# Kernel tuning notes

Measured on AMD Instinct MI355X. Metric: run time of the kernel, lower is better.

## Reference

```python
import jax, jax.numpy as jnp
import numpy as np

M2 = 512  # config['sketch_dim_AV']; seq_len must be divisible by M2


def setup_inputs() -> dict:
    key = jax.random.key(0)
    kq, kk, kv = jax.random.split(key, 3)
    B, H, N, D = 4, 16, 4096, 64
    Q = jax.random.normal(kq, (B, H, N, D), dtype=jnp.float32)
    K = jax.random.normal(kk, (B, H, N, D), dtype=jnp.float32)
    V = jax.random.normal(kv, (B, H, N, D), dtype=jnp.float32)
    mask = jnp.ones((B, N), dtype=jnp.float32)  # unused: self.mask == False
    return {"Q": Q, "K": K, "V": V, "mask": mask}


def reference(Q, K, V, mask):
    # SketchingAttention.forward with sketch_QT=False, method='averaging',
    # sketch_AV=True, use_relu=False, skip_V=True, mask disabled.
    B, H, N, D = Q.shape
    scale = D ** 0.5
    # right_sketch_3D on KS = K.transpose(-1,-2) (shape b,h,d,n):
    # torch does reshape(b*h, d, n) -> reshape(b, h, m2, n//m2, d).mean(-2).
    # Row-major reshape semantics match jnp.reshape exactly, including the
    # intentional (d,n)->(m2, n//m2, d) block reinterpretation.
    SKS = jnp.swapaxes(K, -1, -2).reshape(B, H, M2, N // M2, D).mean(axis=-2)  # (B,H,M2,D)
    # compute_attn(QS, SKS): softmax(Q @ SKS^T / sqrt(d)) over the sketch axis
    logits = jnp.einsum('bhnd,bhmd->bhnm', Q, SKS) / scale  # (B,H,N,M2)
    A_est = jax.nn.softmax(logits, axis=-1)
    # ST_V: chunk-average V along the sequence into M2 buckets
    ST_V = V.reshape(B, H, M2, N // M2, D).mean(axis=-2)  # (B,H,M2,D)
    AV_est = jnp.einsum('bhnm,bhmd->bhnd', A_est, ST_V)
    return AV_est + V  # skip_V residual
```

## Files before the change

### kernel.cpp

```cpp
#include <hip/hip_runtime.h>

using short8 = __attribute__((ext_vector_type(8))) short;
using f32x4  = __attribute__((ext_vector_type(4))) float;

constexpr int NN = 4096;
constexpr int DD = 64;
constexpr int MM = 512;
constexpr int BH = 64;

__device__ __forceinline__ short f2bf(float f) {
    union { float f; unsigned u; } v; v.f = f;
    unsigned r = v.u + 0x7FFF + ((v.u >> 16) & 1);
    return (short)(r >> 16);
}

__global__ __launch_bounds__(1024) void sketch_kernel(
    const float* __restrict__ K, const float* __restrict__ V,
    short* __restrict__ sks, short* __restrict__ stvT) {
    __shared__ float lds[64][65];
    const int t  = threadIdx.x;
    const int lo = t & 63;
    const int hi = t >> 6;
    const int bh = blockIdx.x >> 3;
    const int g  = blockIdx.x & 7;
    const float* Kb = K + ((size_t)bh * NN + g * 512) * DD;
    const float* Vb = V + ((size_t)bh * NN + g * 512) * DD;

#pragma unroll
    for (int i = 0; i < 4; ++i) {
        int e = hi * 4 + i;
        float s = 0.f;
#pragma unroll
        for (int c = 0; c < 8; ++c)
            s += Kb[(size_t)(c * 64 + e) * DD + lo];
        lds[e][lo] = s * 0.125f;
    }
    __syncthreads();
#pragma unroll
    for (int i = 0; i < 4; ++i) {
        int d = hi * 4 + i;
        sks[((size_t)bh * MM + d * 8 + g) * DD + lo] = f2bf(lds[lo][d]);
    }
    __syncthreads();
#pragma unroll
    for (int i = 0; i < 4; ++i) {
        int ml = hi * 4 + i;
        float s = 0.f;
#pragma unroll
        for (int c = 0; c < 8; ++c)
            s += Vb[(size_t)(ml * 8 + c) * DD + lo];
        lds[ml][lo] = s * 0.125f;
    }
    __syncthreads();
#pragma unroll
    for (int i = 0; i < 4; ++i) {
        int e = hi * 4 + i;
        stvT[((size_t)bh * DD + e) * MM + g * 64 + lo] = f2bf(lds[lo][e]);
    }
}

__global__ __launch_bounds__(256, 3) void attn_kernel(
    const float* __restrict__ Q, const float* __restrict__ V,
    const short* __restrict__ sks, const short* __restrict__ stvT,
    float* __restrict__ out) {
    __shared__ __align__(16) short sks_s[64][72];
    __shared__ __align__(16) short stv_s[64][72];
    __shared__ __align__(16) short p_s[4][2][16][72];

    const int tid  = threadIdx.x;
    const int wave = tid >> 6;
    const int lane = tid & 63;
    const int quad = lane >> 4;
    const int l16  = lane & 15;
    const int bh   = blockIdx.x >> 5;
    const int rb   = (blockIdx.x & 31) * 128 + wave * 32;

    const short* sksb = sks + (size_t)bh * MM * DD;
    const short* stvb = stvT + (size_t)bh * DD * MM;

    short8 aq[2][2];
#pragma unroll
    for (int t = 0; t < 2; ++t) {
        const float* qr = Q + ((size_t)bh * NN + rb + t * 16 + l16) * DD;
#pragma unroll
        for (int kc = 0; kc < 2; ++kc)
#pragma unroll
            for (int j = 0; j < 8; ++j)
                aq[t][kc][j] = f2bf(qr[kc * 32 + quad * 8 + j] * 0.125f);
    }

    f32x4 O[2][4];
    float psum[2][4];
#pragma unroll
    for (int t = 0; t < 2; ++t)
#pragma unroll
        for (int nb = 0; nb < 4; ++nb) O[t][nb] = (f32x4){0.f, 0.f, 0.f, 0.f};
#pragma unroll
    for (int t = 0; t < 2; ++t)
#pragma unroll
        for (int r = 0; r < 4; ++r) psum[t][r] = 0.f;

    const int srow = tid >> 2;
    const int scol = (tid & 3) * 16;
    short8 pfk0, pfk1, pfv0, pfv1;
    {
        const short* gk = sksb + (size_t)srow * DD + scol;
        const short* gv = stvb + (size_t)srow * MM + scol;
        pfk0 = *(const short8*)gk;  pfk1 = *(const short8*)(gk + 8);
        pfv0 = *(const short8*)gv;  pfv1 = *(const short8*)(gv + 8);
    }

    for (int mc = 0; mc < 8; ++mc) {
        if (mc) __syncthreads();
        *(short8*)&sks_s[srow][scol]     = pfk0;
        *(short8*)&sks_s[srow][scol + 8] = pfk1;
        *(short8*)&stv_s[srow][scol]     = pfv0;
        *(short8*)&stv_s[srow][scol + 8] = pfv1;
        __syncthreads();
        if (mc < 7) {
            const short* gk = sksb + (size_t)(mc + 1) * 64 * DD + (size_t)srow * DD + scol;
            const short* gv = stvb + (size_t)srow * MM + (mc + 1) * 64 + scol;
            pfk0 = *(const short8*)gk;  pfk1 = *(const short8*)(gk + 8);
            pfv0 = *(const short8*)gv;  pfv1 = *(const short8*)(gv + 8);
        }

        f32x4 S[2][4];
#pragma unroll
        for (int t = 0; t < 2; ++t)
#pragma unroll
            for (int jb = 0; jb < 4; ++jb) S[t][jb] = (f32x4){0.f, 0.f, 0.f, 0.f};
#pragma unroll
        for (int jb = 0; jb < 4; ++jb) {
#pragma unroll
            for (int kc = 0; kc < 2; ++kc) {
                short8 b = *(const short8*)&sks_s[jb * 16 + l16][kc * 32 + quad * 8];
                S[0][jb] = __builtin_amdgcn_mfma_f32_16x16x32_bf16(aq[0][kc], b, S[0][jb], 0, 0, 0);
                S[1][jb] = __builtin_amdgcn_mfma_f32_16x16x32_bf16(aq[1][kc], b, S[1][jb], 0, 0, 0);
            }
        }

#pragma unroll
        for (int t = 0; t < 2; ++t)
#pragma unroll
            for (int jb = 0; jb < 4; ++jb)
#pragma unroll
                for (int r = 0; r < 4; ++r) {
                    float e = __expf(S[t][jb][r]);
                    psum[t][r] += e;
                    p_s[wave][t][quad * 4 + r][jb * 16 + l16] = f2bf(e);
                }

#pragma unroll
        for (int kc = 0; kc < 2; ++kc) {
            short8 a0 = *(const short8*)&p_s[wave][0][l16][kc * 32 + quad * 8];
            short8 a1 = *(const short8*)&p_s[wave][1][l16][kc * 32 + quad * 8];
#pragma unroll
            for (int nb = 0; nb < 4; ++nb) {
                short8 b = *(const short8*)&stv_s[nb * 16 + l16][kc * 32 + quad * 8];
                O[0][nb] = __builtin_amdgcn_mfma_f32_16x16x32_bf16(a0, b, O[0][nb], 0, 0, 0);
                O[1][nb] = __builtin_amdgcn_mfma_f32_16x16x32_bf16(a1, b, O[1][nb], 0, 0, 0);
            }
        }
    }

    float inv[2][4];
#pragma unroll
    for (int t = 0; t < 2; ++t)
#pragma unroll
        for (int r = 0; r < 4; ++r) {
            float s = psum[t][r];
#pragma unroll
            for (int off = 1; off <= 8; off <<= 1)
                s += __shfl_xor(s, off, 64);
            inv[t][r] = 1.0f / s;
        }
#pragma unroll
    for (int t = 0; t < 2; ++t)
#pragma unroll
        for (int nb = 0; nb < 4; ++nb)
#pragma unroll
            for (int r = 0; r < 4; ++r) {
                size_t idx = ((size_t)bh * NN + rb + t * 16 + quad * 4 + r) * DD + nb * 16 + l16;
                out[idx] = O[t][nb][r] * inv[t][r] + V[idx];
            }
}

extern "C" void kernel_launch(void* const* d_in, const int* in_sizes, int n_in,
                              void* d_out, int out_size, void* d_ws, size_t ws_size,
                              hipStream_t stream) {
    const float* Q = (const float*)d_in[0];
    const float* K = (const float*)d_in[1];
    const float* V = (const float*)d_in[2];
    float* out = (float*)d_out;

    short* sks  = (short*)d_ws;
    short* stvT = sks + (size_t)BH * MM * DD;

    sketch_kernel<<<BH * 8, 1024, 0, stream>>>(K, V, sks, stvT);
    attn_kernel<<<BH * (NN / 128), 256, 0, stream>>>(Q, V, sks, stvT, out);
}
```

Measured before the change: 256.3 us.

## Keep softmax probabilities in registers via transposed QK MFMA and permuted STV layout

Computes S transposed by swapping the MFMA operands, so each lane holds consecutive sketch columns for one query row. The exponentials are packed to bf16 with v_cvt_pk_bf16_f32 and fed directly as the A operand of the PV MFMA, which removes the per-wave LDS round trip for P. To match the resulting k ordering, the sketch kernel writes STV^T with a permuted column order. Row sums shrink to two scalars reduced across quads. The launch bound is raised to 4 blocks per CU to allow more occupancy.

```diff
diff --git a/kernel.cpp b/kernel.cpp
--- a/kernel.cpp
+++ b/kernel.cpp
@@ -12,6 +12,12 @@
     union { float f; unsigned u; } v; v.f = f;
     unsigned r = v.u + 0x7FFF + ((v.u >> 16) & 1);
     return (short)(r >> 16);
+}
+
+__device__ __forceinline__ unsigned cvt_pk_bf16(float lo, float hi) {
+    unsigned r;
+    asm("v_cvt_pk_bf16_f32 %0, %1, %2" : "=v"(r) : "v"(lo), "v"(hi));
+    return r;
 }
 
 __global__ __launch_bounds__(1024) void sketch_kernel(
@@ -52,20 +58,20 @@
         lds[ml][lo] = s * 0.125f;
     }
     __syncthreads();
+    const int pm = ((lo & 0x1C) << 1) | ((lo & 0x20) >> 3) | (lo & 3);
 #pragma unroll
     for (int i = 0; i < 4; ++i) {
         int e = hi * 4 + i;
-        stvT[((size_t)bh * DD + e) * MM + g * 64 + lo] = f2bf(lds[lo][e]);
-    }
-}
-
-__global__ __launch_bounds__(256, 3) void attn_kernel(
+        stvT[((size_t)bh * DD + e) * MM + g * 64 + pm] = f2bf(lds[lo][e]);
+    }
+}
+
+__global__ __launch_bounds__(256, 4) void attn_kernel(
     const float* __restrict__ Q, const float* __restrict__ V,
     const short* __restrict__ sks, const short* __restrict__ stvT,
     float* __restrict__ out) {
     __shared__ __align__(16) short sks_s[64][72];
     __shared__ __align__(16) short stv_s[64][72];
-    __shared__ __align__(16) short p_s[4][2][16][72];
 
     const int tid  = threadIdx.x;
     const int wave = tid >> 6;
@@ -90,15 +96,11 @@
     }
 
     f32x4 O[2][4];
-    float psum[2][4];
 #pragma unroll
     for (int t = 0; t < 2; ++t)
 #pragma unroll
         for (int nb = 0; nb < 4; ++nb) O[t][nb] = (f32x4){0.f, 0.f, 0.f, 0.f};
-#pragma unroll
-    for (int t = 0; t < 2; ++t)
-#pragma unroll
-        for (int r = 0; r < 4; ++r) psum[t][r] = 0.f;
+    float psum[2] = {0.f, 0.f};
 
     const int srow = tid >> 2;
     const int scol = (tid & 3) * 16;
@@ -124,65 +126,68 @@
             pfv0 = *(const short8*)gv;  pfv1 = *(const short8*)(gv + 8);
         }
 
-        f32x4 S[2][4];
-#pragma unroll
-        for (int t = 0; t < 2; ++t)
-#pragma unroll
-            for (int jb = 0; jb < 4; ++jb) S[t][jb] = (f32x4){0.f, 0.f, 0.f, 0.f};
+        unsigned pk[2][4][2];
 #pragma unroll
         for (int jb = 0; jb < 4; ++jb) {
+            f32x4 s0 = (f32x4){0.f, 0.f, 0.f, 0.f};
+            f32x4 s1 = (f32x4){0.f, 0.f, 0.f, 0.f};
 #pragma unroll
             for (int kc = 0; kc < 2; ++kc) {
-                short8 b = *(const short8*)&sks_s[jb * 16 + l16][kc * 32 + quad * 8];
-                S[0][jb] = __builtin_amdgcn_mfma_f32_16x16x32_bf16(aq[0][kc], b, S[0][jb], 0, 0, 0);
-                S[1][jb] = __builtin_amdgcn_mfma_f32_16x16x32_bf16(aq[1][kc], b, S[1][jb], 0, 0, 0);
-            }
-        }
-
-#pragma unroll
-        for (int t = 0; t < 2; ++t)
-#pragma unroll
-            for (int jb = 0; jb < 4; ++jb)
-#pragma unroll
-                for (int r = 0; r < 4; ++r) {
-                    float e = __expf(S[t][jb][r]);
-                    psum[t][r] += e;
-                    p_s[wave][t][quad * 4 + r][jb * 16 + l16] = f2bf(e);
-                }
-
-#pragma unroll
-        for (int kc = 0; kc < 2; ++kc) {
-            short8 a0 = *(const short8*)&p_s[wave][0][l16][kc * 32 + quad * 8];
-            short8 a1 = *(const short8*)&p_s[wave][1][l16][kc * 32 + quad * 8];
+                short8 am = *(const short8*)&sks_s[jb * 16 + l16][kc * 32 + quad * 8];
+                s0 = __builtin_amdgcn_mfma_f32_16x16x32_bf16(am, aq[0][kc], s0, 0, 0, 0);
+                s1 = __builtin_amdgcn_mfma_f32_16x16x32_bf16(am, aq[1][kc], s1, 0, 0, 0);
+            }
+#pragma unroll
+            for (int rp = 0; rp < 2; ++rp) {
+                float e0 = __expf(s0[2 * rp]), e1 = __expf(s0[2 * rp + 1]);
+                psum[0] += e0 + e1;
+                pk[0][jb][rp] = cvt_pk_bf16(e0, e1);
+                float f0 = __expf(s1[2 * rp]), f1 = __expf(s1[2 * rp + 1]);
+                psum[1] += f0 + f1;
+                pk[1][jb][rp] = cvt_pk_bf16(f0, f1);
+            }
+        }
+
+        short8 ap[2][2];
+#pragma unroll
+        for (int t = 0; t < 2; ++t) {
+            union { unsigned u[4]; short8 s; } u0, u1;
+            u0.u[0] = pk[t][0][0]; u0.u[1] = pk[t][0][1];
+            u0.u[2] = pk[t][2][0]; u0.u[3] = pk[t][2][1];
+            u1.u[0] = pk[t][1][0]; u1.u[1] = pk[t][1][1];
+            u1.u[2] = pk[t][3][0]; u1.u[3] = pk[t][3][1];
+            ap[t][0] = u0.s; ap[t][1] = u1.s;
+        }
+
+#pragma unroll
+        for (int kc = 0; kc < 2; ++kc)
 #pragma unroll
             for (int nb = 0; nb < 4; ++nb) {
                 short8 b = *(const short8*)&stv_s[nb * 16 + l16][kc * 32 + quad * 8];
-                O[0][nb] = __builtin_amdgcn_mfma_f32_16x16x32_bf16(a0, b, O[0][nb], 0, 0, 0);
-                O[1][nb] = __builtin_amdgcn_mfma_f32_16x16x32_bf16(a1, b, O[1][nb], 0, 0, 0);
-            }
-        }
-    }
-
-    float inv[2][4];
+                O[0][nb] = __builtin_amdgcn_mfma_f32_16x16x32_bf16(ap[0][kc], b, O[0][nb], 0, 0, 0);
+                O[1][nb] = __builtin_amdgcn_mfma_f32_16x16x32_bf16(ap[1][kc], b, O[1][nb], 0, 0, 0);
+            }
+    }
+
+    float inv[2];
+#pragma unroll
+    for (int t = 0; t < 2; ++t) {
+        float s = psum[t];
+        s += __shfl_xor(s, 16);
+        s += __shfl_xor(s, 32);
+        inv[t] = 1.0f / s;
+    }
 #pragma unroll
     for (int t = 0; t < 2; ++t)
 #pragma unroll
         for (int r = 0; r < 4; ++r) {
-            float s = psum[t][r];
-#pragma unroll
-            for (int off = 1; off <= 8; off <<= 1)
-                s += __shfl_xor(s, off, 64);
-            inv[t][r] = 1.0f / s;
-        }
-#pragma unroll
-    for (int t = 0; t < 2; ++t)
-#pragma unroll
-        for (int nb = 0; nb < 4; ++nb)
-#pragma unroll
-            for (int r = 0; r < 4; ++r) {
+            float iv = __shfl(inv[t], quad * 4 + r);
+#pragma unroll
+            for (int nb = 0; nb < 4; ++nb) {
                 size_t idx = ((size_t)bh * NN + rb + t * 16 + quad * 4 + r) * DD + nb * 16 + l16;
-                out[idx] = O[t][nb][r] * inv[t][r] + V[idx];
-            }
+                out[idx] = O[t][nb][r] * iv + V[idx];
+            }
+        }
 }
 
 extern "C" void kernel_launch(void* const* d_in, const int* in_sizes, int n_in,
```

Result: faster. 250.6 us (-2.2%).
